# Performance work log

Measured on AMD Instinct MI355X. Metric: run time of the kernel, lower is better.

## Reference

```python
import jax, jax.numpy as jnp
import numpy as np

C = 256  # in_channels
B, N = 8, 2048


def setup_inputs() -> dict:
    key = jax.random.key(0)
    ks = jax.random.split(key, 9)
    s = 1.0 / np.sqrt(C)  # conv1d default init scale (approx)
    return {
        "x": jax.random.normal(ks[0], (B, C, N), jnp.float32),
        "wq": jax.random.normal(ks[1], (C, C), jnp.float32) * s,
        "bq": jax.random.normal(ks[2], (C,), jnp.float32) * s,
        "wk": jax.random.normal(ks[3], (C, C), jnp.float32) * s,
        "bk": jax.random.normal(ks[4], (C,), jnp.float32) * s,
        "wv": jax.random.normal(ks[5], (C, C), jnp.float32) * s,
        "bv": jax.random.normal(ks[6], (C,), jnp.float32) * s,
        "wo": jax.random.normal(ks[7], (C, C), jnp.float32) * s,
        "bo": jax.random.normal(ks[8], (C,), jnp.float32) * s,
    }


def reference(x, wq, bq, wk, bk, wv, bv, wo, bo):
    # 1x1 Conv1d == channel-wise linear: [C_out,C_in] x [B,C_in,N] -> [B,C_out,N]
    proj = lambda w, b, t: jnp.einsum('ci,bin->bcn', w, t) + b[None, :, None]
    q = proj(wq, bq, x)
    k = proj(wk, bk, x)
    v = proj(wv, bv, x)
    norm = 1.0 / (x.shape[1] ** 0.5)
    # scores: w[b,n,m] = sum_c q[b,c,n] k[b,c,m]
    w = jnp.einsum('bcn,bcm->bnm', q, k) * norm
    w = jax.nn.softmax(w, axis=2)
    # attn output: sum_m v[b,c,m] w[b,n,m] -> [B,C,N]
    av = jnp.einsum('bcm,bnm->bcn', v, w)
    out = proj(wo, bo, av)
    return x + out
```

## Files before the change

### kernel.cpp

```cpp
#include <hip/hip_runtime.h>
#include <hip/hip_bf16.h>

#define CCH 256
#define NSEQ 2048
#define BATCH 8

typedef __hip_bfloat16 bf16;
typedef short s8v __attribute__((ext_vector_type(8)));
typedef float f4v __attribute__((ext_vector_type(4)));
typedef float f16v __attribute__((ext_vector_type(16)));

struct __align__(8) bf16x4 { bf16 v[4]; };

__device__ __forceinline__ float b2f(bf16 h) { return __bfloat162float(h); }
__device__ __forceinline__ bf16 f2b(float f) { return __float2bfloat16(f); }

#define MFMA16(a, b, c) __builtin_amdgcn_mfma_f32_16x16x32_bf16((a), (b), (c), 0, 0, 0)
#define MFMA32(a, b, c) __builtin_amdgcn_mfma_f32_32x32x16_bf16((a), (b), (c), 0, 0, 0)

__device__ __forceinline__ void gload_lds16(const bf16* g, bf16* l) {
    __builtin_amdgcn_global_load_lds(
        (const __attribute__((address_space(1))) unsigned int*)(g),
        (__attribute__((address_space(3))) unsigned int*)(l), 16, 0, 0);
}

__global__ __launch_bounds__(256) void prepw_kernel(
    const float* __restrict__ wq, const float* __restrict__ wk,
    const float* __restrict__ wv, const float* __restrict__ wo,
    bf16* __restrict__ wqb, bf16* __restrict__ wkb,
    bf16* __restrict__ wvb, bf16* __restrict__ wob)
{
    int base = (blockIdx.x * 256 + threadIdx.x) * 8;
    int mat = base >> 16, off = base & 65535;
    const float* s = (mat == 0) ? wq : (mat == 1) ? wk : (mat == 2) ? wv : wo;
    bf16* d = (mat == 0) ? wqb : (mat == 1) ? wkb : (mat == 2) ? wvb : wob;
    int doff = (mat == 3) ? off : (off ^ (((off >> 8) & 7) << 3));
    bf16 tmp[8];
    #pragma unroll
    for (int j = 0; j < 8; ++j) tmp[j] = f2b(s[off + j]);
    *(s8v*)&d[doff] = *(const s8v*)tmp;
}

__global__ __launch_bounds__(512, 6) void qkvprep_kernel(
    const float* __restrict__ x,
    const bf16* __restrict__ Wq, const bf16* __restrict__ Wk,
    const bf16* __restrict__ Wv,
    const float* __restrict__ bq, const float* __restrict__ bk,
    const float* __restrict__ bv,
    bf16* __restrict__ qTt, bf16* __restrict__ kTt, bf16* __restrict__ Vt)
{
    __shared__ bf16 xs[64][260];
    __shared__ bf16 wbuf[2][2][4096];

    const int tile = blockIdx.x;
    const int flat0 = tile * 64;
    const int phase = blockIdx.y;
    const int b = flat0 >> 11, nn = flat0 & 2047;
    const int tid = threadIdx.x;
    const int w = tid >> 6, lane = tid & 63;
    const int l15 = lane & 15, quad = lane >> 4;
    const int ng = w & 3;
    const int ch = w >> 2;
    const float* xb = x + (size_t)b * CCH * NSEQ;

    bf16* qt = qTt + (size_t)tile * 16384;
    bf16* kt = kTt + (size_t)tile * 16384;
    bf16* Vtb = Vt + (size_t)b * CCH * NSEQ;

    const bf16* Wm = (phase == 0) ? Wq : (phase == 1) ? Wk : Wv;
    auto stage = [&](int j, int par) {
        const bf16* src = Wm + (size_t)(ch * 8 + j) * 4096;
        bf16* dst = &wbuf[ch][par][0];
        int seg = (w & 3) * 2;
        gload_lds16(src + (seg + 0) * 512 + lane * 8, dst + (seg + 0) * 512);
        gload_lds16(src + (seg + 1) * 512 + lane * 8, dst + (seg + 1) * 512);
    };

    stage(0, 0);
    #pragma unroll
    for (int i = 0; i < 8; ++i) {
        int f4i = i * 512 + tid;
        int c = f4i >> 4, nq = f4i & 15;
        float4 v4 = *(const float4*)&xb[(size_t)c * NSEQ + nn + nq * 4];
        xs[nq * 4 + 0][c] = f2b(v4.x);
        xs[nq * 4 + 1][c] = f2b(v4.y);
        xs[nq * 4 + 2][c] = f2b(v4.z);
        xs[nq * 4 + 3][c] = f2b(v4.w);
    }
    __syncthreads();

    s8v xf[8];
    #pragma unroll
    for (int t = 0; t < 8; ++t)
        xf[t] = *(const s8v*)&xs[ng * 16 + l15][t * 32 + quad * 8];

    int par = 0;
    #pragma unroll
    for (int j = 0; j < 8; ++j) {
        if (j < 7) stage(j + 1, par ^ 1);

        const char* wb = (const char*)&wbuf[ch][par][0];
        s8v wf[8];
        #pragma unroll
        for (int t = 0; t < 8; ++t)
            wf[t] = *(const s8v*)(wb + l15 * 512 +
                                  ((t * 64 + quad * 16) ^ ((l15 & 7) << 4)));

        const int cs = ch * 8 + j;
        if (phase < 2) {
            f4v a0 = {}, a1 = {};
            #pragma unroll
            for (int t = 0; t < 4; ++t) {
                a0 = MFMA16(wf[t], xf[t], a0);
                a1 = MFMA16(wf[t + 4], xf[t + 4], a1);
            }
            const bool isq = (phase == 0);
            const float* bm = isq ? bq : bk;
            bf16* ot = isq ? qt : kt;
            const float sc = isq ? 0.0625f : 1.0f;
            float4 bb4 = *(const float4*)&bm[cs * 16 + quad * 4];
            float bbr[4] = { bb4.x, bb4.y, bb4.z, bb4.w };
            bf16x4 pk;
            #pragma unroll
            for (int r = 0; r < 4; ++r)
                pk.v[r] = f2b((a0[r] + a1[r] + bbr[r]) * sc);
            int nl = ng * 16 + l15;
            *(bf16x4*)&ot[(cs * 2 + (quad >> 1)) * 512 + nl * 8 + (quad & 1) * 4] = pk;
        } else {
            f4v a0 = {}, a1 = {};
            #pragma unroll
            for (int t = 0; t < 4; ++t) {
                a0 = MFMA16(xf[t], wf[t], a0);
                a1 = MFMA16(xf[t + 4], wf[t + 4], a1);
            }
            int c = cs * 16 + l15;
            float bb = bv[c];
            bf16x4 pk;
            #pragma unroll
            for (int r = 0; r < 4; ++r)
                pk.v[r] = f2b(a0[r] + a1[r] + bb);
            const int m16 = (nn >> 4) + ng;
            size_t e0 = ((size_t)m16 * 256 + c) * 16 + (quad >> 1) * 8 + (quad & 1) * 4;
            *(bf16x4*)&Vtb[e0] = pk;
        }
        __syncthreads();
        par ^= 1;
    }
}

__global__ __launch_bounds__(512, 2) void flash_kernel(
    const bf16* __restrict__ qTt, const bf16* __restrict__ kTt,
    const bf16* __restrict__ Vt, const bf16* __restrict__ Wob,
    const float* __restrict__ bo, const float* __restrict__ x,
    float* __restrict__ out)
{
    __shared__ bf16 Kc[2][16384];
    __shared__ bf16 Ps[2][64][68];
    __shared__ bf16 avs[64][260];
    __shared__ float l_s[4][64];
    __shared__ float ilt[64];

    const int b = blockIdx.x, ntb = blockIdx.y;
    const int tid = threadIdx.x;
    const int W = tid >> 6, lane = tid & 63;
    const int l31 = lane & 31, h = lane >> 5;
    const int ng = W >> 2, mg = (W >> 1) & 1, mu = W & 1;
    const bf16* Vtb = Vt + (size_t)b * CCH * NSEQ;

    s8v qf[16];
    {
        const bf16* qt = qTt + (size_t)(b * 32 + ntb) * 16384;
        #pragma unroll
        for (int t = 0; t < 16; ++t)
            qf[t] = *(const s8v*)&qt[(t * 2 + h) * 512 + (ng * 32 + l31) * 8];
    }
    const bf16* vbase = Vtb + (size_t)(W * 32 + l31) * 16 + h * 8;

    f16v O[2] = {};
    float lsum = 0.f;

    auto stageK2 = [&](int t8) {
        #pragma unroll
        for (int u = 0; u < 2; ++u) {
            const bf16* kt = kTt + (size_t)(b * 32 + t8 * 2 + u) * 16384;
            #pragma unroll
            for (int i = 0; i < 4; ++i) {
                int ch = W * 4 + i;
                gload_lds16(kt + ch * 512 + lane * 8, &Kc[u][ch * 512]);
            }
        }
    };

    stageK2(0);
    __syncthreads();

    for (int t8 = 0; t8 < 16; ++t8) {
        f16v S0 = {}, S1 = {};
        __builtin_amdgcn_s_setprio(1);
        #pragma unroll
        for (int t = 0; t < 8; ++t) {
            s8v kf0 = *(const s8v*)&Kc[mu][(t * 2 + h) * 512 + (mg * 32 + l31) * 8];
            s8v kf1 = *(const s8v*)&Kc[mu][((t + 8) * 2 + h) * 512 + (mg * 32 + l31) * 8];
            S0 = MFMA32(kf0, qf[t], S0);
            S1 = MFMA32(kf1, qf[t + 8], S1);
        }
        __builtin_amdgcn_s_setprio(0);
        s8v vf[2][4];
        #pragma unroll
        for (int u = 0; u < 2; ++u)
            #pragma unroll
            for (int ks = 0; ks < 4; ++ks)
                vf[u][ks] = *(const s8v*)(vbase
                    + (size_t)((t8 * 2 + u) * 4 + ks) * 4096);
        #pragma unroll
        for (int q = 0; q < 4; ++q) {
            bf16x4 pk;
            #pragma unroll
            for (int r = 0; r < 4; ++r) {
                float e = __expf(fminf(S0[q * 4 + r] + S1[q * 4 + r], 60.f));
                lsum += e;
                pk.v[r] = f2b(e);
            }
            *(bf16x4*)&Ps[mu][ng * 32 + l31][mg * 32 + q * 8 + h * 4] = pk;
        }
        __syncthreads();

        if (t8 < 15) stageK2(t8 + 1);

        __builtin_amdgcn_s_setprio(1);
        #pragma unroll
        for (int u = 0; u < 2; ++u)
            #pragma unroll
            for (int ks = 0; ks < 4; ++ks) {
                s8v pf0 = *(const s8v*)&Ps[u][l31][ks * 16 + h * 8];
                s8v pf1 = *(const s8v*)&Ps[u][32 + l31][ks * 16 + h * 8];
                O[0] = MFMA32(vf[u][ks], pf0, O[0]);
                O[1] = MFMA32(vf[u][ks], pf1, O[1]);
            }
        __builtin_amdgcn_s_setprio(0);
        __syncthreads();
    }

    {
        float s = lsum + __shfl_xor(lsum, 32);
        if (h == 0) l_s[mg * 2 + mu][ng * 32 + l31] = s;
    }
    __syncthreads();
    if (tid < 64)
        ilt[tid] = 1.f / (l_s[0][tid] + l_s[1][tid]
                        + l_s[2][tid] + l_s[3][tid]);
    __syncthreads();

    #pragma unroll
    for (int g2 = 0; g2 < 2; ++g2) {
        float il = ilt[g2 * 32 + l31];
        #pragma unroll
        for (int q2 = 0; q2 < 4; ++q2) {
            bf16x4 pk;
            #pragma unroll
            for (int r = 0; r < 4; ++r)
                pk.v[r] = f2b(O[g2][q2 * 4 + r] * il);
            *(bf16x4*)&avs[g2 * 32 + l31][W * 32 + q2 * 8 + 4 * h] = pk;
        }
    }
    __syncthreads();

    const int l15 = lane & 15, quad = lane >> 4;
    const int nn = ntb * 64;
    const size_t base = (size_t)b * CCH * NSEQ;
    #pragma unroll
    for (int cs = 0; cs < 2; ++cs) {
        const int cg = W * 32 + cs * 16;
        s8v af[8];
        #pragma unroll
        for (int t = 0; t < 8; ++t)
            af[t] = *(const s8v*)&Wob[(size_t)(cg + l15) * CCH + t * 32 + quad * 8];
        f4v O4[4] = {};
        #pragma unroll
        for (int nt2 = 0; nt2 < 4; ++nt2)
            #pragma unroll
            for (int t = 0; t < 8; ++t) {
                s8v br = *(const s8v*)&avs[nt2 * 16 + l15][t * 32 + quad * 8];
                O4[nt2] = MFMA16(af[t], br, O4[nt2]);
            }
        #pragma unroll
        for (int r = 0; r < 4; ++r) {
            int c = cg + quad * 4 + r;
            float bb = bo[c];
            #pragma unroll
            for (int nt2 = 0; nt2 < 4; ++nt2) {
                size_t idx = base + (size_t)c * NSEQ + nn + nt2 * 16 + l15;
                out[idx] = O4[nt2][r] + bb + x[idx];
            }
        }
    }
}

extern "C" void kernel_launch(void* const* d_in, const int* in_sizes, int n_in,
                              void* d_out, int out_size, void* d_ws, size_t ws_size,
                              hipStream_t stream) {
    (void)in_sizes; (void)n_in; (void)out_size; (void)ws_size;
    const float* x  = (const float*)d_in[0];
    const float* wq = (const float*)d_in[1];
    const float* bq = (const float*)d_in[2];
    const float* wk = (const float*)d_in[3];
    const float* bk = (const float*)d_in[4];
    const float* wv = (const float*)d_in[5];
    const float* bv = (const float*)d_in[6];
    const float* wo = (const float*)d_in[7];
    const float* bo = (const float*)d_in[8];
    float* out = (float*)d_out;

    const size_t T = (size_t)BATCH * CCH * NSEQ;
    bf16* qTt  = (bf16*)d_ws;
    bf16* kTt  = qTt + T;
    bf16* Vt   = kTt + T;
    bf16* wqb  = Vt + T;
    bf16* wkb  = wqb + 65536;
    bf16* wvb  = wkb + 65536;
    bf16* wob  = wvb + 65536;

    prepw_kernel<<<128, 256, 0, stream>>>(wq, wk, wv, wo, wqb, wkb, wvb, wob);
    qkvprep_kernel<<<dim3(256, 3), 512, 0, stream>>>(
        x, wqb, wkb, wvb, bq, bk, bv, qTt, kTt, Vt);
    flash_kernel<<<dim3(8, 32), 512, 0, stream>>>(
        qTt, kTt, Vt, wob, bo, x, out);
}
```

Measured before the change: 156.7 us.

## Split flash blocks to 32 query rows and merge QKV projection into two phases

```diff
diff --git a/kernel.cpp b/kernel.cpp
--- a/kernel.cpp
+++ b/kernel.cpp
@@ -41,7 +41,7 @@
     *(s8v*)&d[doff] = *(const s8v*)tmp;
 }
 
-__global__ __launch_bounds__(512, 6) void qkvprep_kernel(
+__global__ __launch_bounds__(512, 4) void qkvprep_kernel(
     const float* __restrict__ x,
     const bf16* __restrict__ Wq, const bf16* __restrict__ Wk,
     const bf16* __restrict__ Wv,
@@ -67,9 +67,16 @@
     bf16* kt = kTt + (size_t)tile * 16384;
     bf16* Vtb = Vt + (size_t)b * CCH * NSEQ;
 
-    const bf16* Wm = (phase == 0) ? Wq : (phase == 1) ? Wk : Wv;
+    auto chunk_ptr = [&](int j) -> const bf16* {
+        if (phase == 0)
+            return (j < 8) ? Wq + (size_t)(ch * 8 + j) * 4096
+                           : Wk + (size_t)(ch * 4 + (j - 8)) * 4096;
+        else
+            return (j < 8) ? Wv + (size_t)(ch * 8 + j) * 4096
+                           : Wk + (size_t)(8 + ch * 4 + (j - 8)) * 4096;
+    };
     auto stage = [&](int j, int par) {
-        const bf16* src = Wm + (size_t)(ch * 8 + j) * 4096;
+        const bf16* src = chunk_ptr(j);
         bf16* dst = &wbuf[ch][par][0];
         int seg = (w & 3) * 2;
         gload_lds16(src + (seg + 0) * 512 + lane * 8, dst + (seg + 0) * 512);
@@ -96,8 +103,8 @@
 
     int par = 0;
     #pragma unroll
-    for (int j = 0; j < 8; ++j) {
-        if (j < 7) stage(j + 1, par ^ 1);
+    for (int j = 0; j < 12; ++j) {
+        if (j < 11) stage(j + 1, par ^ 1);
 
         const char* wb = (const char*)&wbuf[ch][par][0];
         s8v wf[8];
@@ -106,15 +113,17 @@
             wf[t] = *(const s8v*)(wb + l15 * 512 +
                                   ((t * 64 + quad * 16) ^ ((l15 & 7) << 4)));
 
-        const int cs = ch * 8 + j;
-        if (phase < 2) {
+        if (phase == 0 || j >= 8) {
             f4v a0 = {}, a1 = {};
             #pragma unroll
             for (int t = 0; t < 4; ++t) {
                 a0 = MFMA16(wf[t], xf[t], a0);
                 a1 = MFMA16(wf[t + 4], xf[t + 4], a1);
             }
-            const bool isq = (phase == 0);
+            const bool isq = (phase == 0) && (j < 8);
+            const int cs = (phase == 0)
+                ? (j < 8 ? ch * 8 + j : ch * 4 + (j - 8))
+                : (8 + ch * 4 + (j - 8));
             const float* bm = isq ? bq : bk;
             bf16* ot = isq ? qt : kt;
             const float sc = isq ? 0.0625f : 1.0f;
@@ -133,6 +142,7 @@
                 a0 = MFMA16(xf[t], wf[t], a0);
                 a1 = MFMA16(xf[t + 4], wf[t + 4], a1);
             }
+            const int cs = ch * 8 + j;
             int c = cs * 16 + l15;
             float bb = bv[c];
             bf16x4 pk;
@@ -148,46 +158,44 @@
     }
 }
 
-__global__ __launch_bounds__(512, 2) void flash_kernel(
+__global__ __launch_bounds__(256, 2) void flash_kernel(
     const bf16* __restrict__ qTt, const bf16* __restrict__ kTt,
     const bf16* __restrict__ Vt, const bf16* __restrict__ Wob,
     const float* __restrict__ bo, const float* __restrict__ x,
     float* __restrict__ out)
 {
     __shared__ bf16 Kc[2][16384];
-    __shared__ bf16 Ps[2][64][68];
-    __shared__ bf16 avs[64][260];
-    __shared__ float l_s[4][64];
-    __shared__ float ilt[64];
+    __shared__ bf16 Ps[2][32][68];
+    __shared__ float l_s[4][32];
+    __shared__ float ilt[32];
 
     const int b = blockIdx.x, ntb = blockIdx.y;
     const int tid = threadIdx.x;
     const int W = tid >> 6, lane = tid & 63;
     const int l31 = lane & 31, h = lane >> 5;
-    const int ng = W >> 2, mg = (W >> 1) & 1, mu = W & 1;
+    const int mu = W & 1, mg = W >> 1;
     const bf16* Vtb = Vt + (size_t)b * CCH * NSEQ;
 
     s8v qf[16];
     {
-        const bf16* qt = qTt + (size_t)(b * 32 + ntb) * 16384;
+        const bf16* qt = qTt + (size_t)(b * 32 + (ntb >> 1)) * 16384;
+        const int r0 = (ntb & 1) * 32;
         #pragma unroll
         for (int t = 0; t < 16; ++t)
-            qf[t] = *(const s8v*)&qt[(t * 2 + h) * 512 + (ng * 32 + l31) * 8];
-    }
-    const bf16* vbase = Vtb + (size_t)(W * 32 + l31) * 16 + h * 8;
+            qf[t] = *(const s8v*)&qt[(t * 2 + h) * 512 + (r0 + l31) * 8];
+    }
+    const bf16* vbase = Vtb + (size_t)(W * 64 + l31) * 16 + h * 8;
 
     f16v O[2] = {};
     float lsum = 0.f;
 
     auto stageK2 = [&](int t8) {
         #pragma unroll
-        for (int u = 0; u < 2; ++u) {
+        for (int i = 0; i < 16; ++i) {
+            int s = W * 16 + i;
+            int u = s >> 5, ch = s & 31;
             const bf16* kt = kTt + (size_t)(b * 32 + t8 * 2 + u) * 16384;
-            #pragma unroll
-            for (int i = 0; i < 4; ++i) {
-                int ch = W * 4 + i;
-                gload_lds16(kt + ch * 512 + lane * 8, &Kc[u][ch * 512]);
-            }
+            gload_lds16(kt + ch * 512 + lane * 8, &Kc[u][ch * 512]);
         }
     };
 
@@ -205,13 +213,13 @@
             S1 = MFMA32(kf1, qf[t + 8], S1);
         }
         __builtin_amdgcn_s_setprio(0);
-        s8v vf[2][4];
-        #pragma unroll
-        for (int u = 0; u < 2; ++u)
-            #pragma unroll
-            for (int ks = 0; ks < 4; ++ks)
-                vf[u][ks] = *(const s8v*)(vbase
-                    + (size_t)((t8 * 2 + u) * 4 + ks) * 4096);
+        s8v vf0[2][4];
+        #pragma unroll
+        for (int ks = 0; ks < 4; ++ks)
+            #pragma unroll
+            for (int cr = 0; cr < 2; ++cr)
+                vf0[cr][ks] = *(const s8v*)(vbase
+                    + (size_t)((t8 * 2 + 0) * 4 + ks) * 4096 + cr * 512);
         #pragma unroll
         for (int q = 0; q < 4; ++q) {
             bf16x4 pk;
@@ -221,66 +229,78 @@
                 lsum += e;
                 pk.v[r] = f2b(e);
             }
-            *(bf16x4*)&Ps[mu][ng * 32 + l31][mg * 32 + q * 8 + h * 4] = pk;
+            *(bf16x4*)&Ps[mu][l31][mg * 32 + q * 8 + h * 4] = pk;
         }
         __syncthreads();
 
         if (t8 < 15) stageK2(t8 + 1);
+        s8v vf1[2][4];
+        #pragma unroll
+        for (int ks = 0; ks < 4; ++ks)
+            #pragma unroll
+            for (int cr = 0; cr < 2; ++cr)
+                vf1[cr][ks] = *(const s8v*)(vbase
+                    + (size_t)((t8 * 2 + 1) * 4 + ks) * 4096 + cr * 512);
 
         __builtin_amdgcn_s_setprio(1);
         #pragma unroll
-        for (int u = 0; u < 2; ++u)
-            #pragma unroll
-            for (int ks = 0; ks < 4; ++ks) {
-                s8v pf0 = *(const s8v*)&Ps[u][l31][ks * 16 + h * 8];
-                s8v pf1 = *(const s8v*)&Ps[u][32 + l31][ks * 16 + h * 8];
-                O[0] = MFMA32(vf[u][ks], pf0, O[0]);
-                O[1] = MFMA32(vf[u][ks], pf1, O[1]);
-            }
+        for (int ks = 0; ks < 4; ++ks) {
+            s8v pf = *(const s8v*)&Ps[0][l31][ks * 16 + h * 8];
+            O[0] = MFMA32(vf0[0][ks], pf, O[0]);
+            O[1] = MFMA32(vf0[1][ks], pf, O[1]);
+        }
+        #pragma unroll
+        for (int ks = 0; ks < 4; ++ks) {
+            s8v pf = *(const s8v*)&Ps[1][l31][ks * 16 + h * 8];
+            O[0] = MFMA32(vf1[0][ks], pf, O[0]);
+            O[1] = MFMA32(vf1[1][ks], pf, O[1]);
+        }
         __builtin_amdgcn_s_setprio(0);
         __syncthreads();
     }
 
     {
         float s = lsum + __shfl_xor(lsum, 32);
-        if (h == 0) l_s[mg * 2 + mu][ng * 32 + l31] = s;
-    }
-    __syncthreads();
-    if (tid < 64)
+        if (h == 0) l_s[W][l31] = s;
+    }
+    __syncthreads();
+    if (tid < 32)
         ilt[tid] = 1.f / (l_s[0][tid] + l_s[1][tid]
                         + l_s[2][tid] + l_s[3][tid]);
     __syncthreads();
 
-    #pragma unroll
-    for (int g2 = 0; g2 < 2; ++g2) {
-        float il = ilt[g2 * 32 + l31];
-        #pragma unroll
-        for (int q2 = 0; q2 < 4; ++q2) {
-            bf16x4 pk;
-            #pragma unroll
-            for (int r = 0; r < 4; ++r)
-                pk.v[r] = f2b(O[g2][q2 * 4 + r] * il);
-            *(bf16x4*)&avs[g2 * 32 + l31][W * 32 + q2 * 8 + 4 * h] = pk;
-        }
+    bf16* avs = &Kc[0][0];
+    {
+        float il = ilt[l31];
+        #pragma unroll
+        for (int cr = 0; cr < 2; ++cr)
+            #pragma unroll
+            for (int q2 = 0; q2 < 4; ++q2) {
+                bf16x4 pk;
+                #pragma unroll
+                for (int r = 0; r < 4; ++r)
+                    pk.v[r] = f2b(O[cr][q2 * 4 + r] * il);
+                *(bf16x4*)&avs[l31 * 260 + W * 64 + cr * 32 + q2 * 8 + 4 * h] = pk;
+            }
     }
     __syncthreads();
 
     const int l15 = lane & 15, quad = lane >> 4;
-    const int nn = ntb * 64;
+    const int nn = ntb * 32;
     const size_t base = (size_t)b * CCH * NSEQ;
     #pragma unroll
-    for (int cs = 0; cs < 2; ++cs) {
-        const int cg = W * 32 + cs * 16;
+    for (int cs = 0; cs < 4; ++cs) {
+        const int cg = W * 64 + cs * 16;
         s8v af[8];
         #pragma unroll
         for (int t = 0; t < 8; ++t)
             af[t] = *(const s8v*)&Wob[(size_t)(cg + l15) * CCH + t * 32 + quad * 8];
-        f4v O4[4] = {};
-        #pragma unroll
-        for (int nt2 = 0; nt2 < 4; ++nt2)
+        f4v O4[2] = {};
+        #pragma unroll
+        for (int nt2 = 0; nt2 < 2; ++nt2)
             #pragma unroll
             for (int t = 0; t < 8; ++t) {
-                s8v br = *(const s8v*)&avs[nt2 * 16 + l15][t * 32 + quad * 8];
+                s8v br = *(const s8v*)&avs[(nt2 * 16 + l15) * 260 + t * 32 + quad * 8];
                 O4[nt2] = MFMA16(af[t], br, O4[nt2]);
             }
         #pragma unroll
@@ -288,7 +308,7 @@
             int c = cg + quad * 4 + r;
             float bb = bo[c];
             #pragma unroll
-            for (int nt2 = 0; nt2 < 4; ++nt2) {
+            for (int nt2 = 0; nt2 < 2; ++nt2) {
                 size_t idx = base + (size_t)c * NSEQ + nn + nt2 * 16 + l15;
                 out[idx] = O4[nt2][r] + bb + x[idx];
             }
@@ -321,8 +341,8 @@
     bf16* wob  = wvb + 65536;
 
     prepw_kernel<<<128, 256, 0, stream>>>(wq, wk, wv, wo, wqb, wkb, wvb, wob);
-    qkvprep_kernel<<<dim3(256, 3), 512, 0, stream>>>(
+    qkvprep_kernel<<<dim3(256, 2), 512, 0, stream>>>(
         x, wqb, wkb, wvb, bq, bk, bv, qTt, kTt, Vt);
-    flash_kernel<<<dim3(8, 32), 512, 0, stream>>>(
+    flash_kernel<<<dim3(8, 64), 256, 0, stream>>>(
         qTt, kTt, Vt, wob, bo, x, out);
 }
```

Measured after the change: 165.6 us. 1.06x slower.
